# Kernel tuning notes

Measured on AMD Instinct MI355X. Metric: run time of the kernel, lower is better.

## Reference

```python
import jax, jax.numpy as jnp
import numpy as np

N, E, D, R = 50000, 600000, 128, 8


def rgcn_conv(x, ei, et, W, root, bias):
    # PyG RGCNConv with aggr='mean', root_weight=True, bias=True.
    src, dst = ei[0], ei[1]
    # per-relation transform of all node features: [N, R, D]
    xw = jnp.einsum('nd,rde->nre', x, W)
    msg = xw[src, et]                      # [E, D] gather per edge
    seg = dst * R + et                     # segment per (node, relation)
    summed = jax.ops.segment_sum(msg, seg, num_segments=N * R)
    cnt = jax.ops.segment_sum(jnp.ones((msg.shape[0],), x.dtype), seg,
                              num_segments=N * R)
    mean = summed / jnp.maximum(cnt, 1.0)[:, None]
    agg = mean.reshape(N, R, D).sum(axis=1)  # sum over relations
    return agg + x @ root + bias


def setup_inputs() -> dict:
    key = jax.random.key(0)
    ks = jax.random.split(key, 9)
    s = 1.0 / np.sqrt(D)
    x = jax.random.normal(ks[0], (N, D), jnp.float32)
    ei = jax.random.randint(ks[1], (2, E), 0, N, jnp.int32)
    et = jax.random.randint(ks[2], (E,), 0, R, jnp.int32)
    W1 = jax.random.normal(ks[3], (R, D, D), jnp.float32) * s
    root1 = jax.random.normal(ks[4], (D, D), jnp.float32) * s
    b1 = jnp.zeros((D,), jnp.float32)
    W2 = jax.random.normal(ks[5], (R, D, D), jnp.float32) * s
    root2 = jax.random.normal(ks[6], (D, D), jnp.float32) * s
    b2 = jnp.zeros((D,), jnp.float32)
    rel_emb = jax.random.normal(ks[7], (R, D), jnp.float32)
    return {"x": x, "ei": ei, "et": et, "W1": W1, "root1": root1, "b1": b1,
            "W2": W2, "root2": root2, "b2": b2, "rel_emb": rel_emb}


def reference(x, ei, et, W1, root1, b1, W2, root2, b2, rel_emb):
    h = jax.nn.relu(rgcn_conv(x, ei, et, W1, root1, b1))
    h = jax.nn.relu(rgcn_conv(h, ei, et, W2, root2, b2))
    return (h, rel_emb)
```

## Files before the change

kernel.cpp:

```cpp
#include <hip/hip_runtime.h>
#include <stdint.h>

#define N_NODES 50000
#define N_EDGES 600000
#define N_REL   8
#define KDIM    1152
#define KA      1024
#define NPAD    50048
#define RCAP    16

typedef short v8s __attribute__((ext_vector_type(8)));
typedef float v4f __attribute__((ext_vector_type(4)));
typedef unsigned short u16;
typedef unsigned int   u32;
typedef __attribute__((address_space(1))) const u32 gas_u32;
typedef __attribute__((address_space(3))) u32 las_u32;

__device__ __forceinline__ float bf2f(u16 u) {
    union { u32 i; float f; } t; t.i = ((u32)u) << 16; return t.f;
}
__device__ __forceinline__ u16 f2bf(float f) {
    union { float f; u32 i; } t; t.f = f;
    u32 lsb = (t.i >> 16) & 1u;
    t.i += 0x7fffu + lsb;
    return (u16)(t.i >> 16);
}
__device__ __forceinline__ float load_f(const void* p, int i, int fl) {
    return fl ? bf2f(((const u16*)p)[i]) : ((const float*)p)[i];
}
__device__ __forceinline__ int wave_detect(const u32* __restrict__ x32) {
    u32 w = x32[threadIdx.x & 63];
    u32 e = (w >> 7) & 0xffu;
    unsigned long long m = __ballot(e >= 112u && e < 144u);
    return __popcll(m) >= 32;
}

#define B_CF    2344
#define B_CONV  (B_CF + 3125)
#define B_PREPW (B_CONV + 1153)
#define B_RELEMB (B_PREPW + 4)
__global__ void k_prep(const void* __restrict__ x, const int* __restrict__ ei,
                       const int* __restrict__ et,
                       const void* __restrict__ W1, const void* __restrict__ r1,
                       const void* __restrict__ b1, const void* __restrict__ W2,
                       const void* __restrict__ r2, const void* __restrict__ b2,
                       const void* __restrict__ rel_emb,
                       u16* __restrict__ xc, u16* __restrict__ Wbig,
                       u16* __restrict__ bc, int* __restrict__ cnt,
                       u16* __restrict__ evalF, void* __restrict__ out) {
    int b = blockIdx.x, tid = threadIdx.x;
    int fl = wave_detect((const u32*)x);
    if (b < B_CF) {
        int i = b * 256 + tid;
        if (i < N_EDGES) {
            int d = ei[N_EDGES + i];
            int bkt = d * N_REL + et[i];
            int pos = atomicAdd(&cnt[bkt], 1);
            if (pos < RCAP) evalF[(size_t)bkt * RCAP + pos] = (u16)ei[i];
        }
    } else if (b < B_CONV) {
        int g = (b - B_CF) * 256 + tid;
        if (fl) {
            ((int4*)xc)[g] = ((const int4*)x)[g];
        } else {
            const float* xf = (const float*)x + g * 8;
            u16 o[8];
            #pragma unroll
            for (int j = 0; j < 8; ++j) o[j] = f2bf(xf[j]);
            *(int4*)(xc + g * 8) = *(const int4*)o;
        }
    } else if (b < B_PREPW) {
        int o = (b - B_CONV) * 256 + tid;
        if (o < 2 * 128 * KDIM) {
            int l = o / (128 * KDIM);
            int rem = o - l * (128 * KDIM);
            int j = rem / KDIM, k = rem - j * KDIM;
            float v;
            if (k < 1024) {
                int r = k >> 7, kk = k & 127;
                v = load_f(l ? W2 : W1, r * 16384 + kk * 128 + j, fl);
            } else {
                v = load_f(l ? r2 : r1, (k - 1024) * 128 + j, fl);
            }
            Wbig[o] = f2bf(v);
        } else if (o < 2 * 128 * KDIM + 256) {
            int o2 = o - 2 * 128 * KDIM;
            bc[o2] = f2bf(load_f((o2 >> 7) ? b2 : b1, o2 & 127, fl));
        }
    } else {
        int i = (b - B_PREPW) * 256 + tid;
        if (i < N_REL * 128) {
            size_t o = (size_t)N_NODES * 128 + i;
            if (fl) ((u16*)out)[o]   = ((const u16*)rel_emb)[i];
            else    ((float*)out)[o] = ((const float*)rel_emb)[i];
        }
    }
}

__global__ __launch_bounds__(256) void k_agg_all(
        const u16* __restrict__ feat,
        const int* __restrict__ cnt, const u16* __restrict__ evalF,
        u16* __restrict__ aggAll) {
    int wave = threadIdx.x >> 6, lane = threadIdx.x & 63;
    int node = blockIdx.x * 4 + wave;
    if (node >= N_NODES) return;
    int c2 = lane * 2;
    int base = node * N_REL;
    int4 ca = ((const int4*)(cnt + base))[0];
    int4 cb = ((const int4*)(cnt + base))[1];
    int cs[8] = {ca.x, ca.y, ca.z, ca.w, cb.x, cb.y, cb.z, cb.w};
    const u16* ep0 = evalF + (size_t)base * RCAP;
    u16* d = aggAll + (size_t)node * KA + c2;
    #pragma unroll
    for (int r = 0; r < N_REL; ++r) {
        int c = cs[r]; if (c > RCAP) c = RCAP;
        const u16* ep = ep0 + r * RCAP;
        float sx = 0.f, sy = 0.f;
        int i = 0;
        for (; i + 3 < c; i += 4) {
            ushort4 s4 = *(const ushort4*)(ep + i);
            ushort2 u0 = *(const ushort2*)(feat + ((size_t)s4.x << 7) + c2);
            ushort2 u1 = *(const ushort2*)(feat + ((size_t)s4.y << 7) + c2);
            ushort2 u2 = *(const ushort2*)(feat + ((size_t)s4.z << 7) + c2);
            ushort2 u3 = *(const ushort2*)(feat + ((size_t)s4.w << 7) + c2);
            sx += bf2f(u0.x) + bf2f(u1.x) + bf2f(u2.x) + bf2f(u3.x);
            sy += bf2f(u0.y) + bf2f(u1.y) + bf2f(u2.y) + bf2f(u3.y);
        }
        for (; i < c; ++i) {
            int s0 = ep[i];
            ushort2 u0 = *(const ushort2*)(feat + ((size_t)s0 << 7) + c2);
            sx += bf2f(u0.x); sy += bf2f(u0.y);
        }
        float inv = __builtin_amdgcn_rcpf((float)(c > 0 ? c : 1));
        ushort2 o; o.x = f2bf(sx * inv); o.y = f2bf(sy * inv);
        *(ushort2*)(d + r * 128) = o;
    }
}

__global__ __launch_bounds__(512, 4) void k_gemm(
        const u16* __restrict__ A,
        const u16* __restrict__ feat,
        const u16* __restrict__ Bw,
        const u16* __restrict__ bias,
        const u32* __restrict__ xdet,
        u16* __restrict__ hout, void* __restrict__ fout,
        int final_out) {
    __shared__ __align__(16) u16 As[128 * 128];
    __shared__ __align__(16) u16 Bs[128 * 128];
    int tid = threadIdx.x;
    int fl = wave_detect(xdet);
    int bm0 = blockIdx.x * 128;
    int wave = tid >> 6, lane = tid & 63;
    int wm = (wave & 3) * 32, wn = (wave >> 2) * 64;
    int lrow = lane & 15, quad = lane >> 4;

    v4f accr[2][4];
    #pragma unroll
    for (int i = 0; i < 2; ++i)
        #pragma unroll
        for (int j = 0; j < 4; ++j) accr[i][j] = (v4f){0.f, 0.f, 0.f, 0.f};

    for (int h = 0; h < 9; ++h) {
        if (h) __syncthreads();
        #pragma unroll
        for (int j = 0; j < 4; ++j) {
            int off = wave * 4096 + j * 1024 + lane * 16;
            int row = off >> 8;
            int swz = (off >> 4) & 15;
            int cc = swz ^ (row & 15);
            const u16* srcA = (h < 8)
                ? A + (size_t)(bm0 + row) * KA + h * 128 + cc * 8
                : feat + (size_t)(bm0 + row) * 128 + cc * 8;
            __builtin_amdgcn_global_load_lds((gas_u32*)srcA,
                (las_u32*)(As + (off >> 1) - lane * 8), 16, 0, 0);
            __builtin_amdgcn_global_load_lds(
                (gas_u32*)(Bw + (size_t)row * KDIM + h * 128 + cc * 8),
                (las_u32*)(Bs + (off >> 1) - lane * 8), 16, 0, 0);
        }
        __syncthreads();

        #pragma unroll
        for (int kk = 0; kk < 4; ++kk) {
            int chunk = kk * 4 + quad;
            v8s a[2], b[4];
            #pragma unroll
            for (int t = 0; t < 2; ++t) {
                int row = wm + t * 16 + lrow;
                a[t] = *(const v8s*)(As + row * 128 + (chunk ^ (row & 15)) * 8);
            }
            #pragma unroll
            for (int t = 0; t < 4; ++t) {
                int row = wn + t * 16 + lrow;
                b[t] = *(const v8s*)(Bs + row * 128 + (chunk ^ (row & 15)) * 8);
            }
            #pragma unroll
            for (int ti = 0; ti < 2; ++ti)
                #pragma unroll
                for (int tj = 0; tj < 4; ++tj)
                    accr[ti][tj] = __builtin_amdgcn_mfma_f32_16x16x32_bf16(a[ti], b[tj], accr[ti][tj], 0, 0, 0);
        }
    }

    #pragma unroll
    for (int ti = 0; ti < 2; ++ti)
        #pragma unroll
        for (int reg = 0; reg < 4; ++reg) {
            int gm = bm0 + wm + ti * 16 + quad * 4 + reg;
            if (gm >= N_NODES) continue;
            #pragma unroll
            for (int tj = 0; tj < 4; ++tj) {
                int col = wn + tj * 16 + lrow;
                size_t idx = (size_t)gm * 128 + col;
                float v = fmaxf(accr[ti][tj][reg] + bf2f(bias[col]), 0.f);
                if (!final_out) hout[idx] = f2bf(v);
                else if (fl)    ((u16*)fout)[idx] = f2bf(v);
                else            ((float*)fout)[idx] = v;
            }
        }
}

static inline size_t align_up(size_t x, size_t a) { return (x + a - 1) & ~(a - 1); }

extern "C" void kernel_launch(void* const* d_in, const int* in_sizes, int n_in,
                              void* d_out, int out_size, void* d_ws, size_t ws_size,
                              hipStream_t stream) {
    const int* ei = (const int*)d_in[1];
    const int* et = (const int*)d_in[2];

    char* ws = (char*)d_ws;
    size_t off = 0;
    u16* Wbig   = (u16*)(ws + off);  off = align_up(off + (size_t)2 * 128 * KDIM * 2, 256);
    u16* bc     = (u16*)(ws + off);  off = align_up(off + 512, 256);
    u16* xc     = (u16*)(ws + off);  off = align_up(off + (size_t)N_NODES * 128 * 2, 256);
    int* cnt    = (int*)(ws + off);  off = align_up(off + (size_t)N_NODES * N_REL * 4, 256);
    u16* evalF  = (u16*)(ws + off);  off = align_up(off + (size_t)N_NODES * N_REL * RCAP * 2, 256);
    u16* h      = (u16*)(ws + off);  off = align_up(off + (size_t)N_NODES * 128 * 2, 256);
    u16* aggAll = (u16*)(ws + off);  off += (size_t)NPAD * KA * 2;
    (void)in_sizes; (void)n_in; (void)out_size; (void)ws_size;

    hipMemsetAsync(cnt, 0, (size_t)N_NODES * N_REL * 4, stream);
    k_prep<<<B_RELEMB, 256, 0, stream>>>(d_in[0], ei, et, d_in[3], d_in[4], d_in[5],
                                         d_in[6], d_in[7], d_in[8], d_in[9],
                                         xc, Wbig, bc, cnt, evalF, d_out);

    for (int l = 0; l < 2; ++l) {
        const u16* src = l ? h : xc;
        k_agg_all<<<(N_NODES + 3) / 4, 256, 0, stream>>>(src, cnt, evalF, aggAll);
        k_gemm<<<NPAD / 128, 512, 0, stream>>>(aggAll, src, Wbig + (size_t)l * 128 * KDIM,
                                               bc + l * 128, (const u32*)d_in[0],
                                               h, d_out, l);
    }
}
```

Baseline: 296.8 us.

## Fuse neighbor mean aggregation into GEMM A-tile staging, drop aggAll buffer

Removes the separate aggregation kernel and its large intermediate buffer. The GEMM kernel now gathers and averages neighbor features per relation straight into the swizzled LDS A tile for each K-chunk. To keep those reads contiguous, the bucket arrays are transposed to relation-major (rel*NPAD+node). This saves the global write and re-read of the 1024-wide aggregated matrix and one launch per layer. In exchange, irregular gather latency now sits inside the GEMM loop and is not overlapped with the MFMA work.

```diff
diff --git a/kernel.cpp b/kernel.cpp
--- a/kernel.cpp
+++ b/kernel.cpp
@@ -5,7 +5,6 @@
 #define N_EDGES 600000
 #define N_REL   8
 #define KDIM    1152
-#define KA      1024
 #define NPAD    50048
 #define RCAP    16
 
@@ -46,17 +45,17 @@
                        const void* __restrict__ r2, const void* __restrict__ b2,
                        const void* __restrict__ rel_emb,
                        u16* __restrict__ xc, u16* __restrict__ Wbig,
-                       u16* __restrict__ bc, int* __restrict__ cnt,
-                       u16* __restrict__ evalF, void* __restrict__ out) {
+                       u16* __restrict__ bc, int* __restrict__ cntT,
+                       u16* __restrict__ evalT, void* __restrict__ out) {
     int b = blockIdx.x, tid = threadIdx.x;
     int fl = wave_detect((const u32*)x);
     if (b < B_CF) {
         int i = b * 256 + tid;
         if (i < N_EDGES) {
             int d = ei[N_EDGES + i];
-            int bkt = d * N_REL + et[i];
-            int pos = atomicAdd(&cnt[bkt], 1);
-            if (pos < RCAP) evalF[(size_t)bkt * RCAP + pos] = (u16)ei[i];
+            int bkt = et[i] * NPAD + d;
+            int pos = atomicAdd(&cntT[bkt], 1);
+            if (pos < RCAP) evalT[(size_t)bkt * RCAP + pos] = (u16)ei[i];
         }
     } else if (b < B_CONV) {
         int g = (b - B_CF) * 256 + tid;
@@ -97,49 +96,10 @@
     }
 }
 
-__global__ __launch_bounds__(256) void k_agg_all(
+__global__ __launch_bounds__(512, 4) void k_gemm(
         const u16* __restrict__ feat,
-        const int* __restrict__ cnt, const u16* __restrict__ evalF,
-        u16* __restrict__ aggAll) {
-    int wave = threadIdx.x >> 6, lane = threadIdx.x & 63;
-    int node = blockIdx.x * 4 + wave;
-    if (node >= N_NODES) return;
-    int c2 = lane * 2;
-    int base = node * N_REL;
-    int4 ca = ((const int4*)(cnt + base))[0];
-    int4 cb = ((const int4*)(cnt + base))[1];
-    int cs[8] = {ca.x, ca.y, ca.z, ca.w, cb.x, cb.y, cb.z, cb.w};
-    const u16* ep0 = evalF + (size_t)base * RCAP;
-    u16* d = aggAll + (size_t)node * KA + c2;
-    #pragma unroll
-    for (int r = 0; r < N_REL; ++r) {
-        int c = cs[r]; if (c > RCAP) c = RCAP;
-        const u16* ep = ep0 + r * RCAP;
-        float sx = 0.f, sy = 0.f;
-        int i = 0;
-        for (; i + 3 < c; i += 4) {
-            ushort4 s4 = *(const ushort4*)(ep + i);
-            ushort2 u0 = *(const ushort2*)(feat + ((size_t)s4.x << 7) + c2);
-            ushort2 u1 = *(const ushort2*)(feat + ((size_t)s4.y << 7) + c2);
-            ushort2 u2 = *(const ushort2*)(feat + ((size_t)s4.z << 7) + c2);
-            ushort2 u3 = *(const ushort2*)(feat + ((size_t)s4.w << 7) + c2);
-            sx += bf2f(u0.x) + bf2f(u1.x) + bf2f(u2.x) + bf2f(u3.x);
-            sy += bf2f(u0.y) + bf2f(u1.y) + bf2f(u2.y) + bf2f(u3.y);
-        }
-        for (; i < c; ++i) {
-            int s0 = ep[i];
-            ushort2 u0 = *(const ushort2*)(feat + ((size_t)s0 << 7) + c2);
-            sx += bf2f(u0.x); sy += bf2f(u0.y);
-        }
-        float inv = __builtin_amdgcn_rcpf((float)(c > 0 ? c : 1));
-        ushort2 o; o.x = f2bf(sx * inv); o.y = f2bf(sy * inv);
-        *(ushort2*)(d + r * 128) = o;
-    }
-}
-
-__global__ __launch_bounds__(512, 4) void k_gemm(
-        const u16* __restrict__ A,
-        const u16* __restrict__ feat,
+        const int* __restrict__ cntT,
+        const u16* __restrict__ evalT,
         const u16* __restrict__ Bw,
         const u16* __restrict__ bias,
         const u32* __restrict__ xdet,
@@ -153,6 +113,8 @@
     int wave = tid >> 6, lane = tid & 63;
     int wm = (wave & 3) * 32, wn = (wave >> 2) * 64;
     int lrow = lane & 15, quad = lane >> 4;
+    int r0 = wave * 16;
+    int c2 = lane * 2;
 
     v4f accr[2][4];
     #pragma unroll
@@ -166,16 +128,61 @@
         for (int j = 0; j < 4; ++j) {
             int off = wave * 4096 + j * 1024 + lane * 16;
             int row = off >> 8;
-            int swz = (off >> 4) & 15;
-            int cc = swz ^ (row & 15);
-            const u16* srcA = (h < 8)
-                ? A + (size_t)(bm0 + row) * KA + h * 128 + cc * 8
-                : feat + (size_t)(bm0 + row) * 128 + cc * 8;
-            __builtin_amdgcn_global_load_lds((gas_u32*)srcA,
-                (las_u32*)(As + (off >> 1) - lane * 8), 16, 0, 0);
+            int cc = ((off >> 4) & 15) ^ (row & 15);
             __builtin_amdgcn_global_load_lds(
                 (gas_u32*)(Bw + (size_t)row * KDIM + h * 128 + cc * 8),
                 (las_u32*)(Bs + (off >> 1) - lane * 8), 16, 0, 0);
+        }
+        if (h < 8) {
+            const int* cb = cntT + h * NPAD + bm0 + r0;
+            const u16* eb = evalT + ((size_t)(h * NPAD + bm0 + r0)) * RCAP;
+            #pragma unroll
+            for (int g = 0; g < 2; ++g) {
+                int cg[8]; ushort4 eg[8];
+                #pragma unroll
+                for (int rr = 0; rr < 8; ++rr) {
+                    cg[rr] = cb[g * 8 + rr];
+                    eg[rr] = *(const ushort4*)(eb + (size_t)(g * 8 + rr) * RCAP);
+                }
+                #pragma unroll
+                for (int rr = 0; rr < 8; ++rr) {
+                    int row = r0 + g * 8 + rr;
+                    int c = cg[rr] < RCAP ? cg[rr] : RCAP;
+                    int s0 = c > 0 ? (int)eg[rr].x : 0;
+                    int s1 = c > 1 ? (int)eg[rr].y : 0;
+                    int s2 = c > 2 ? (int)eg[rr].z : 0;
+                    int s3 = c > 3 ? (int)eg[rr].w : 0;
+                    ushort2 g0 = *(const ushort2*)(feat + ((size_t)s0 << 7) + c2);
+                    ushort2 g1 = *(const ushort2*)(feat + ((size_t)s1 << 7) + c2);
+                    ushort2 g2 = *(const ushort2*)(feat + ((size_t)s2 << 7) + c2);
+                    ushort2 g3 = *(const ushort2*)(feat + ((size_t)s3 << 7) + c2);
+                    float sx = (c > 0 ? bf2f(g0.x) : 0.f) + (c > 1 ? bf2f(g1.x) : 0.f)
+                             + (c > 2 ? bf2f(g2.x) : 0.f) + (c > 3 ? bf2f(g3.x) : 0.f);
+                    float sy = (c > 0 ? bf2f(g0.y) : 0.f) + (c > 1 ? bf2f(g1.y) : 0.f)
+                             + (c > 2 ? bf2f(g2.y) : 0.f) + (c > 3 ? bf2f(g3.y) : 0.f);
+                    if (c > 4) {
+                        for (int j2 = 4; j2 < c; ++j2) {
+                            int sj = eb[(size_t)(g * 8 + rr) * RCAP + j2];
+                            ushort2 gj = *(const ushort2*)(feat + ((size_t)sj << 7) + c2);
+                            sx += bf2f(gj.x); sy += bf2f(gj.y);
+                        }
+                    }
+                    float inv = __builtin_amdgcn_rcpf((float)(c > 0 ? c : 1));
+                    ushort2 o; o.x = f2bf(sx * inv); o.y = f2bf(sy * inv);
+                    int unit = (lane >> 2) ^ (row & 15);
+                    *(ushort2*)((char*)As + row * 256 + unit * 16 + (lane & 3) * 4) = o;
+                }
+            }
+        } else {
+            #pragma unroll
+            for (int j = 0; j < 4; ++j) {
+                int off = wave * 4096 + j * 1024 + lane * 16;
+                int row = off >> 8;
+                int cc = ((off >> 4) & 15) ^ (row & 15);
+                __builtin_amdgcn_global_load_lds(
+                    (gas_u32*)(feat + (size_t)(bm0 + row) * 128 + cc * 8),
+                    (las_u32*)(As + (off >> 1) - lane * 8), 16, 0, 0);
+            }
         }
         __syncthreads();
 
@@ -231,22 +238,21 @@
     size_t off = 0;
     u16* Wbig   = (u16*)(ws + off);  off = align_up(off + (size_t)2 * 128 * KDIM * 2, 256);
     u16* bc     = (u16*)(ws + off);  off = align_up(off + 512, 256);
-    u16* xc     = (u16*)(ws + off);  off = align_up(off + (size_t)N_NODES * 128 * 2, 256);
-    int* cnt    = (int*)(ws + off);  off = align_up(off + (size_t)N_NODES * N_REL * 4, 256);
-    u16* evalF  = (u16*)(ws + off);  off = align_up(off + (size_t)N_NODES * N_REL * RCAP * 2, 256);
-    u16* h      = (u16*)(ws + off);  off = align_up(off + (size_t)N_NODES * 128 * 2, 256);
-    u16* aggAll = (u16*)(ws + off);  off += (size_t)NPAD * KA * 2;
+    u16* xc     = (u16*)(ws + off);  off = align_up(off + (size_t)NPAD * 128 * 2, 256);
+    int* cntT   = (int*)(ws + off);  off = align_up(off + (size_t)N_REL * NPAD * 4, 256);
+    u16* evalT  = (u16*)(ws + off);  off = align_up(off + (size_t)N_REL * NPAD * RCAP * 2, 256);
+    u16* h      = (u16*)(ws + off);  off = align_up(off + (size_t)NPAD * 128 * 2, 256);
     (void)in_sizes; (void)n_in; (void)out_size; (void)ws_size;
 
-    hipMemsetAsync(cnt, 0, (size_t)N_NODES * N_REL * 4, stream);
+    hipMemsetAsync(cntT, 0, (size_t)N_REL * NPAD * 4, stream);
     k_prep<<<B_RELEMB, 256, 0, stream>>>(d_in[0], ei, et, d_in[3], d_in[4], d_in[5],
                                          d_in[6], d_in[7], d_in[8], d_in[9],
-                                         xc, Wbig, bc, cnt, evalF, d_out);
+                                         xc, Wbig, bc, cntT, evalT, d_out);
 
     for (int l = 0; l < 2; ++l) {
         const u16* src = l ? h : xc;
-        k_agg_all<<<(N_NODES + 3) / 4, 256, 0, stream>>>(src, cnt, evalF, aggAll);
-        k_gemm<<<NPAD / 128, 512, 0, stream>>>(aggAll, src, Wbig + (size_t)l * 128 * KDIM,
+        k_gemm<<<NPAD / 128, 512, 0, stream>>>(src, cntT, evalT,
+                                               Wbig + (size_t)l * 128 * KDIM,
                                                bc + l * 128, (const u32*)d_in[0],
                                                h, d_out, l);
     }
```

Measured after the change: 376.0 us. +26.7%, slower.
